# Performance work log

Hardware: AMD Instinct MI355X
Metric: run time of the kernel (lower is better)

## Reference

```python
import jax, jax.numpy as jnp
import numpy as np
from jax import lax

C, H, W, A = 256, 128, 128, 9
STRIDE = 16
BIG_NEG = -1e9
IOU_THR = 0.7
MIN_SIZE = 16.0


def _make_anchors(h, w, stride):
    scales = np.array([128.0, 256.0, 512.0])
    ratios = np.array([0.5, 1.0, 2.0])
    ah = (scales[:, None] * np.sqrt(ratios)[None, :]).reshape(-1)  # (9,)
    aw = (scales[:, None] / np.sqrt(ratios)[None, :]).reshape(-1)
    cy = (np.arange(h) + 0.5) * stride
    cx = (np.arange(w) + 0.5) * stride
    CY, CX = np.meshgrid(cy, cx, indexing='ij')
    anch = np.stack([
        np.broadcast_to(CY[..., None], (h, w, A)),
        np.broadcast_to(CX[..., None], (h, w, A)),
        np.broadcast_to(ah, (h, w, A)),
        np.broadcast_to(aw, (h, w, A)),
    ], axis=-1)  # (h, w, A, 4) as [cy, cx, h, w]
    return anch.reshape(h, w, A * 4).astype(np.float32)


def _conv(x, w, b):
    y = lax.conv_general_dilated(x, w, (1, 1), 'SAME',
                                 dimension_numbers=('NCHW', 'OIHW', 'NCHW'))
    return y + b[None, :, None, None]


def _iou_one_vs_all(box, boxes):
    # box: (4,) [y1,x1,y2,x2]; boxes: (N,4)
    yy1 = jnp.maximum(box[0], boxes[:, 0])
    xx1 = jnp.maximum(box[1], boxes[:, 1])
    yy2 = jnp.minimum(box[2], boxes[:, 2])
    xx2 = jnp.minimum(box[3], boxes[:, 3])
    inter = jnp.clip(yy2 - yy1, 0.0) * jnp.clip(xx2 - xx1, 0.0)
    a1 = (box[2] - box[0]) * (box[3] - box[1])
    a2 = (boxes[:, 2] - boxes[:, 0]) * (boxes[:, 3] - boxes[:, 1])
    return inter / (a1 + a2 - inter + 1e-9)


def _nms(boxes, scores, k):
    # Greedy NMS: k sequential argmax+suppress steps (jit-safe, fixed shapes).
    def step(s, _):
        i = jnp.argmax(s)
        valid = s[i] > BIG_NEG / 2
        iou = _iou_one_vs_all(boxes[i], boxes)
        s2 = jnp.where(iou > IOU_THR, BIG_NEG, s).at[i].set(BIG_NEG)
        return s2, (i, valid)
    _, (idxs, valids) = lax.scan(step, scores, None, length=k)
    return idxs, valids


def _rpn_forward(x, anchors, conv1_w, conv1_b, cls_w, cls_b, bbox_w, bbox_b,
                 image_h, image_w, before_n, after_n):
    h = jax.nn.relu(_conv(x, conv1_w, conv1_b))
    scores = jax.nn.sigmoid(_conv(h, cls_w, cls_b))          # (1, A, H, W)
    regs = _conv(h, bbox_w, bbox_b)                          # (1, 4A, H, W)
    scores_nhwc = jnp.transpose(scores, (0, 2, 3, 1))        # (1, H, W, A)
    regs_nhwc = jnp.transpose(regs, (0, 2, 3, 1))            # (1, H, W, 4A)

    anchors_flat = anchors.reshape(-1, 4)                    # (N, 4) [cy,cx,h,w]
    s_flat = scores_nhwc.reshape(-1)                         # (N,)
    d_flat = lax.stop_gradient(regs_nhwc.reshape(-1, 4))     # detach, as in torch

    # bbox decode (means=0, stds=1)
    cy = anchors_flat[:, 0] + d_flat[:, 0] * anchors_flat[:, 2]
    cx = anchors_flat[:, 1] + d_flat[:, 1] * anchors_flat[:, 3]
    bh = anchors_flat[:, 2] * jnp.exp(d_flat[:, 2])
    bw = anchors_flat[:, 3] * jnp.exp(d_flat[:, 3])
    props = jnp.stack([cy - 0.5 * bh, cx - 0.5 * bw,
                       cy + 0.5 * bh, cx + 0.5 * bw], axis=-1)  # (N,4) corners

    order = jnp.argsort(-s_flat)[:before_n]                  # top-N by score desc
    boxes = props[order]
    s_top = s_flat[order]

    # clip to image
    boxes = jnp.stack([jnp.clip(boxes[:, 0], 0.0),
                       jnp.clip(boxes[:, 1], 0.0),
                       jnp.minimum(boxes[:, 2], float(image_h)),
                       jnp.minimum(boxes[:, 3], float(image_w))], axis=-1)

    # size filter (>=16 in both dims): mask out via BIG_NEG score
    bh2 = boxes[:, 2] - boxes[:, 0]
    bw2 = boxes[:, 3] - boxes[:, 1]
    s_top = jnp.where((bh2 >= MIN_SIZE) & (bw2 >= MIN_SIZE), s_top, BIG_NEG)

    idxs, valids = _nms(boxes, s_top, after_n)
    out_boxes = boxes[idxs] * valids[:, None].astype(boxes.dtype)  # (after_n, 4)
    return scores_nhwc, regs_nhwc, out_boxes


def setup_inputs() -> dict:
    key = jax.random.key(0)
    k = jax.random.split(key, 4)
    x = jax.random.normal(k[0], (1, C, H, W), jnp.float32)
    conv1_w = 0.01 * jax.random.normal(k[1], (C, C, 3, 3), jnp.float32)
    conv1_b = jnp.zeros((C,), jnp.float32)
    cls_w = 0.01 * jax.random.normal(k[2], (A, C, 1, 1), jnp.float32)
    cls_b = jnp.zeros((A,), jnp.float32)
    bbox_w = 0.01 * jax.random.normal(k[3], (4 * A, C, 1, 1), jnp.float32)
    bbox_b = jnp.zeros((4 * A,), jnp.float32)
    anchors = jnp.asarray(_make_anchors(H, W, STRIDE))
    anchors_valid_map = jnp.ones((H, W, A), jnp.int32)
    return dict(x=x, anchors=anchors, conv1_w=conv1_w, conv1_b=conv1_b,
                cls_w=cls_w, cls_b=cls_b, bbox_w=bbox_w, bbox_b=bbox_b,
                anchors_valid_map=anchors_valid_map,
                image_h=2048, image_w=2048,
                before_proposal_num=6000, after_proposal_num=300)


def reference(x, anchors, conv1_w, conv1_b, cls_w, cls_b, bbox_w, bbox_b,
              anchors_valid_map, image_h, image_w,
              before_proposal_num, after_proposal_num):
    # exclude_edge_proposals=False -> anchors_valid_map unused (no boolean mask)
    return _rpn_forward(x, anchors, conv1_w, conv1_b, cls_w, cls_b,
                        bbox_w, bbox_b, image_h, image_w,
                        before_proposal_num, after_proposal_num)
```

## Files before the change

### kernel.cpp

```cpp
#include <hip/hip_runtime.h>
#include <cmath>

#define NN 147456
#define NPX 16384
#define NB 6000
#define NA 300
#define MW 94
#define EXPB 0x3FEu

__global__ __launch_bounds__(256) void prep_w_k(const float* __restrict__ w, float* __restrict__ wT2,
                                                unsigned int* __restrict__ ghist, unsigned int* __restrict__ cnt,
                                                unsigned long long* __restrict__ flagsG) {
    if (blockIdx.x == 0) {
        for (int i = threadIdx.x; i < 4096; i += 256) ghist[i] = 0;
        if (threadIdx.x == 0) cnt[0] = 0;
        if (threadIdx.x < MW) flagsG[threadIdx.x] = 0ULL;
    }
    int idx = blockIdx.x * 256 + threadIdx.x;
    if (idx >= 2304 * 256) return;
    int co = idx / 2304;
    int k  = idx - co * 2304;
    wT2[k * 256 + co] = w[idx];
}

__global__ __launch_bounds__(128, 2) void conv3_k(const float* __restrict__ x, const float* __restrict__ wT2,
                                                  const float* __restrict__ bias, double* __restrict__ h64) {
    __shared__ double xd[800];
    __shared__ __align__(16) float wl[4608];
    const int bx = blockIdx.x;
    const int tile = ((bx >> 5) << 3) | (bx & 7);
    const int g = (bx >> 3) & 3;
    const int ty0 = (tile >> 4) << 3;
    const int tx0 = (tile & 15) << 3;
    const int tid = threadIdx.x;
    const int qc = tid & 15;
    const int py = tid >> 4;
    const int wv = tid >> 6;
    const int lane = tid & 63;

    int xga[7]; bool xin[7], xwr[7];
    #pragma unroll
    for (int r = 0; r < 7; ++r) {
        int l = tid + r * 128;
        xwr[r] = (l < 800);
        int ci = l / 100; int rem = l - ci * 100;
        int rr = rem / 10; int cc = rem - rr * 10;
        int gy = ty0 + rr - 1, gx = tx0 + cc - 1;
        xin[r] = xwr[r] && gy >= 0 && gy < 128 && gx >= 0 && gx < 128;
        xga[r] = ci * NPX + gy * 128 + gx;
    }
    const float* wbase = wT2 + (g << 6);
    int wsrc[9];
    #pragma unroll
    for (int r = 0; r < 9; ++r) {
        int f = wv * 64 + lane + r * 128;
        wsrc[r] = ((f >> 4) << 8) + ((f & 15) << 2);
    }

    double acc[4][8];
    #pragma unroll
    for (int a = 0; a < 4; ++a)
        #pragma unroll
        for (int b = 0; b < 8; ++b) acc[a][b] = 0.0;

    float xf[7];
    #pragma unroll
    for (int r = 0; r < 7; ++r) { float v = 0.f; if (xin[r]) v = x[xga[r]]; xf[r] = v; }

    for (int ch = 0; ch < 32; ++ch) {
        const float* wp = wbase + ch * 18432;
        __syncthreads();
        #pragma unroll
        for (int r = 0; r < 7; ++r) {
            int l = tid + r * 128;
            if (l < 800) xd[l] = (double)xf[r];
        }
        #pragma unroll
        for (int r = 0; r < 9; ++r) {
            __builtin_amdgcn_global_load_lds(
                (const __attribute__((address_space(1))) unsigned int*)(wp + wsrc[r]),
                (__attribute__((address_space(3))) unsigned int*)&wl[(wv * 64 + r * 128) << 2],
                16, 0, 0);
        }
        __syncthreads();
        if (ch < 31) {
            const int xoff = (ch + 1) * (8 * NPX);
            #pragma unroll
            for (int r = 0; r < 7; ++r) { float v = 0.f; if (xin[r]) v = x[xoff + xga[r]]; xf[r] = v; }
        }
        for (int ci = 0; ci < 8; ++ci) {
            #pragma unroll
            for (int dy = 0; dy < 3; ++dy) {
                double xr[10];
                #pragma unroll
                for (int jj = 0; jj < 5; ++jj) {
                    double2 t = *(const double2*)&xd[ci * 100 + (py + dy) * 10 + 2 * jj];
                    xr[2 * jj] = t.x; xr[2 * jj + 1] = t.y;
                }
                #pragma unroll
                for (int dx = 0; dx < 3; ++dx) {
                    float4 wq = *(const float4*)&wl[((ci * 9 + dy * 3 + dx) << 6) + (qc << 2)];
                    double wvv[4];
                    wvv[0] = (double)wq.x; wvv[1] = (double)wq.y;
                    wvv[2] = (double)wq.z; wvv[3] = (double)wq.w;
                    #pragma unroll
                    for (int co = 0; co < 4; ++co)
                        #pragma unroll
                        for (int p = 0; p < 8; ++p)
                            acc[co][p] = fma(wvv[co], xr[p + dx], acc[co][p]);
                }
            }
        }
    }
    const int oy = ty0 + py;
    #pragma unroll
    for (int co = 0; co < 4; ++co) {
        int oc = (g << 6) + (qc << 2) + co;
        double b = (double)bias[oc];
        #pragma unroll
        for (int p = 0; p < 8; ++p) {
            double v = acc[co][p] + b;
            h64[(size_t)oc * NPX + oy * 128 + tx0 + p] = v > 0.0 ? v : 0.0;
        }
    }
}

__global__ __launch_bounds__(1024) void heads_k(const double* __restrict__ h64,
        const float* __restrict__ cls_w, const float* __restrict__ cls_b,
        const float* __restrict__ bbox_w, const float* __restrict__ bbox_b,
        float* __restrict__ out_scores, float* __restrict__ out_regs,
        double* __restrict__ scores64, double* __restrict__ regs64,
        unsigned int* __restrict__ ghist) {
    __shared__ float wlh[45 * 256];
    __shared__ unsigned int lh[4096];
    const int tid = threadIdx.x;
    for (int l = tid; l < 45 * 256; l += 1024)
        wlh[l] = (l < 2304) ? cls_w[l] : bbox_w[l - 2304];
    for (int i = tid; i < 4096; i += 1024) lh[i] = 0;
    __syncthreads();
    const int w = tid >> 6;
    const int lane = tid & 63;
    const int px = blockIdx.x * 64 + lane;
    const int o0 = w, o1 = w + 16, o2 = w + 32;
    const bool has2 = (o2 < 45);
    double a0 = 0.0, a1 = 0.0, a2 = 0.0;
    const float* w0 = wlh + o0 * 256;
    const float* w1 = wlh + o1 * 256;
    const float* w2 = wlh + (has2 ? o2 : 0) * 256;
    for (int c = 0; c < 256; ++c) {
        double hv = h64[(size_t)c * NPX + px];
        a0 = fma(hv, (double)w0[c], a0);
        a1 = fma(hv, (double)w1[c], a1);
        if (has2) a2 = fma(hv, (double)w2[c], a2);
    }
    auto emit = [&](int o, double acc) {
        if (o < 9) {
            acc += (double)cls_b[o];
            double s = 1.0 / (1.0 + exp(-acc));
            out_scores[px * 9 + o] = (float)s;
            scores64[px * 9 + o] = s;
            unsigned long long bits = (unsigned long long)__double_as_longlong(s);
            if ((unsigned int)(bits >> 52) == EXPB)
                atomicAdd(&lh[(unsigned int)(bits >> 40) & 0xFFFu], 1u);
        } else {
            acc += (double)bbox_b[o - 9];
            out_regs[px * 36 + (o - 9)] = (float)acc;
            regs64[px * 36 + (o - 9)] = acc;
        }
    };
    emit(o0, a0);
    emit(o1, a1);
    if (has2) emit(o2, a2);
    __syncthreads();
    for (int i = tid; i < 4096; i += 1024) {
        unsigned int v = lh[i];
        if (v) atomicAdd(&ghist[i], v);
    }
}

__global__ __launch_bounds__(1024) void gather_k(const double* __restrict__ s64, const unsigned int* __restrict__ ghist,
                                                 unsigned int* __restrict__ counter, unsigned int* __restrict__ cand,
                                                 unsigned long long* __restrict__ ckey) {
    __shared__ unsigned int lcnt, lbase, cutSh;
    const int tid = threadIdx.x;
    if (tid == 0) lcnt = 0;
    if (tid < 64) {
        const int lane = tid;
        unsigned int v[64];
        #pragma unroll
        for (int j = 0; j < 64; ++j) v[j] = ghist[j * 64 + lane];
        unsigned int Tl = 0;
        #pragma unroll
        for (int j = 0; j < 64; ++j) {
            unsigned int s = v[j];
            #pragma unroll
            for (int d = 1; d < 64; d <<= 1) s += __shfl_xor(s, d);
            if (lane == j) Tl = s;
        }
        unsigned int Suf = Tl;
        #pragma unroll
        for (int d = 1; d < 64; d <<= 1) { unsigned int o = __shfl_down(Suf, d); if (lane < 64 - d) Suf += o; }
        unsigned long long m = __ballot(Suf >= (unsigned int)NB);
        if (m == 0ULL) {
            if (lane == 0) cutSh = 0;
        } else {
            const int jstar = 63 - __builtin_clzll(m);
            const unsigned int above_rows = (jstar < 63) ? __shfl(Suf, jstar + 1) : 0u;
            unsigned int hrow = 0;
            #pragma unroll
            for (int j = 0; j < 64; ++j) if (j == jstar) hrow = v[j];
            unsigned int D = hrow;
            #pragma unroll
            for (int d = 1; d < 64; d <<= 1) { unsigned int o = __shfl_down(D, d); if (lane < 64 - d) D += o; }
            unsigned long long m2 = __ballot(above_rows + D >= (unsigned int)NB);
            const int lstar = 63 - __builtin_clzll(m2);
            if (lane == 0) cutSh = (unsigned int)(64 * jstar + lstar);
        }
    }
    __syncthreads();
    const unsigned int T24 = (EXPB << 12) | cutSh;
    const int gid = blockIdx.x * 1024 + tid;
    unsigned long long bits = (unsigned long long)__double_as_longlong(s64[gid]);
    unsigned int k24 = (unsigned int)(bits >> 40);
    unsigned int pos = 0;
    const bool take = (k24 >= T24);
    if (take) pos = atomicAdd(&lcnt, 1u);
    __syncthreads();
    if (tid == 0) lbase = lcnt ? atomicAdd(counter, lcnt) : 0u;
    __syncthreads();
    if (take) {
        unsigned int p = lbase + pos;
        if (p < 8192) { cand[p] = (unsigned int)gid; ckey[p] = bits; }
    }
}

__global__ __launch_bounds__(256) void rank2_k(const unsigned long long* __restrict__ ckey,
        const unsigned int* __restrict__ cand, const unsigned int* __restrict__ counter,
        const float* __restrict__ anchors, const double* __restrict__ r64,
        double* __restrict__ boxes64, unsigned long long* __restrict__ flagsG) {
    int M = (int)*counter; if (M > 8192) M = 8192;
    const int wid = (blockIdx.x * 256 + threadIdx.x) >> 6;
    const int lane = threadIdx.x & 63;
    if (wid >= M) return;
    const unsigned long long myk = ckey[wid];
    const unsigned int myv = cand[wid];
    int cntv = 0;
    int l = lane;
    for (; l + 192 < M; l += 256) {
        unsigned long long k0 = ckey[l], k1 = ckey[l + 64], k2 = ckey[l + 128], k3 = ckey[l + 192];
        unsigned int v0 = cand[l], v1 = cand[l + 64], v2 = cand[l + 128], v3 = cand[l + 192];
        cntv += (k0 > myk || (k0 == myk && v0 < myv));
        cntv += (k1 > myk || (k1 == myk && v1 < myv));
        cntv += (k2 > myk || (k2 == myk && v2 < myv));
        cntv += (k3 > myk || (k3 == myk && v3 < myv));
    }
    for (; l < M; l += 64) {
        unsigned long long kk = ckey[l];
        unsigned int vv = cand[l];
        cntv += (kk > myk || (kk == myk && vv < myv));
    }
    #pragma unroll
    for (int dd = 32; dd; dd >>= 1) cntv += __shfl_down(cntv, dd);
    if (lane == 0 && cntv < NB) {
        const int rk = cntv;
        const int i = (int)myv;
        const int px = i / 9, a = i - 9 * px;
        const float* an = anchors + px * 36 + a * 4;
        const double* d = r64 + px * 36 + a * 4;
        const double acy = (double)an[0], acx = (double)an[1], ah = (double)an[2], aw = (double)an[3];
        const double cy = acy + d[0] * ah;
        const double cx = acx + d[1] * aw;
        const double bh = ah * exp(d[2]);
        const double bw = aw * exp(d[3]);
        double y1 = cy - 0.5 * bh, x1 = cx - 0.5 * bw;
        double y2 = cy + 0.5 * bh, x2 = cx + 0.5 * bw;
        y1 = fmax(y1, 0.0); x1 = fmax(x1, 0.0);
        y2 = fmin(y2, 2048.0); x2 = fmin(x2, 2048.0);
        boxes64[rk * 4 + 0] = y1; boxes64[rk * 4 + 1] = x1;
        boxes64[rk * 4 + 2] = y2; boxes64[rk * 4 + 3] = x2;
        if (((y2 - y1) >= 16.0) && ((x2 - x1) >= 16.0))
            atomicOr(&flagsG[rk >> 6], 1ULL << (rk & 63));
    }
}

__global__ __launch_bounds__(64) void iou_k(const double* __restrict__ boxes64, unsigned long long* __restrict__ mask) {
    const int bi = blockIdx.x, bj = blockIdx.y;
    const int t = threadIdx.x;
    const int i = bi * 64 + t;
    if (bj < bi) {
        if (i < NB) mask[(size_t)i * MW + bj] = 0ULL;
        return;
    }
    __shared__ double jb[64][4];
    const int j0 = bj * 64;
    const int jn = min(64, NB - j0);
    if (t < jn) {
        jb[t][0] = boxes64[(j0 + t) * 4 + 0];
        jb[t][1] = boxes64[(j0 + t) * 4 + 1];
        jb[t][2] = boxes64[(j0 + t) * 4 + 2];
        jb[t][3] = boxes64[(j0 + t) * 4 + 3];
    }
    __syncthreads();
    if (i >= NB) return;
    const double y1 = boxes64[i * 4 + 0], x1 = boxes64[i * 4 + 1];
    const double y2 = boxes64[i * 4 + 2], x2 = boxes64[i * 4 + 3];
    const double a1 = (y2 - y1) * (x2 - x1);
    unsigned long long wbits = 0ULL;
    for (int jj = 0; jj < jn; ++jj) {
        const int j = j0 + jj;
        if (j <= i) continue;
        const double yy1 = fmax(y1, jb[jj][0]);
        const double xx1 = fmax(x1, jb[jj][1]);
        const double yy2 = fmin(y2, jb[jj][2]);
        const double xx2 = fmin(x2, jb[jj][3]);
        const double ih = fmax(yy2 - yy1, 0.0);
        const double iw = fmax(xx2 - xx1, 0.0);
        const double inter = ih * iw;
        const double a2 = (jb[jj][2] - jb[jj][0]) * (jb[jj][3] - jb[jj][1]);
        const double iou = inter / (a1 + a2 - inter + 1e-9);
        if (iou > 0.7) wbits |= (1ULL << jj);
    }
    mask[(size_t)i * MW + bj] = wbits;
}

__global__ __launch_bounds__(64) void nms_k(const double* __restrict__ boxes64,
                                            const unsigned long long* __restrict__ flagsG,
                                            const unsigned long long* __restrict__ mask, float* __restrict__ out_boxes) {
    __shared__ unsigned long long flags[MW], supp[MW];
    const int lane = threadIdx.x;
    for (int w = lane; w < MW; w += 64) { flags[w] = flagsG[w]; supp[w] = 0ULL; }
    __syncthreads();
    int nk = 0;
    for (int w = 0; w < MW && nk < NA; ++w) {
        unsigned long long done = 0ULL;
        const bool loWord = (w < 64);
        const int holder = loWord ? w : (w - 64);
        for (;;) {
            if (nk >= NA) break;
            unsigned long long avail = flags[w] & ~supp[w] & ~done;
            if (!avail) break;
            int b[16]; int n = 0;
            unsigned long long t = avail;
            #pragma unroll
            for (int q = 0; q < 16; ++q) {
                if (t) { b[q] = __builtin_ctzll(t); t &= t - 1; n = q + 1; }
                else   { b[q] = 0; }
            }
            unsigned long long dmask = 0ULL;
            #pragma unroll
            for (int q = 0; q < 16; ++q) if (q < n) dmask |= 1ULL << b[q];
            done |= dmask;
            unsigned long long r0[16], r1[16];
            #pragma unroll
            for (int q = 0; q < 16; ++q) {
                int cq = w * 64 + ((q < n) ? b[q] : b[0]);
                r0[q] = mask[(size_t)cq * MW + lane];
                r1[q] = (lane + 64 < MW) ? mask[(size_t)cq * MW + lane + 64] : 0ULL;
            }
            double bxv;
            {
                int q = lane >> 2;
                int cq = w * 64 + ((q < n) ? b[q] : b[0]);
                bxv = boxes64[(size_t)cq * 4 + (lane & 3)];
            }
            unsigned km[15];
            #pragma unroll
            for (int qp = 0; qp < 15; ++qp) {
                unsigned m = 0;
                if (qp + 1 < n) {
                    unsigned long long wordq = __shfl(loWord ? r0[qp] : r1[qp], holder);
                    #pragma unroll
                    for (int q = 1; q < 16; ++q)
                        if (q > qp) m |= ((unsigned)((wordq >> b[q]) & 1ULL)) << q;
                }
                km[qp] = m;
            }
            unsigned selm = 1u;
            #pragma unroll
            for (int q = 1; q < 16; ++q) {
                if (q < n) {
                    unsigned kb = 0;
                    #pragma unroll
                    for (int qp = 0; qp < 15; ++qp)
                        if (qp < q) kb |= ((km[qp] >> q) & 1u) << qp;
                    if ((kb & selm) == 0u) selm |= (1u << q);
                }
            }
            int outpos[16]; int nsel = 0;
            #pragma unroll
            for (int q = 0; q < 16; ++q) { outpos[q] = nk + nsel; if (q < n && ((selm >> q) & 1u)) ++nsel; }
            {
                int q = lane >> 2;
                if (q < n && ((selm >> q) & 1u) && outpos[q] < NA)
                    out_boxes[outpos[q] * 4 + (lane & 3)] = (float)bxv;
            }
            unsigned long long o0 = 0ULL, o1 = 0ULL;
            #pragma unroll
            for (int q = 0; q < 16; ++q)
                if (q < n && ((selm >> q) & 1u)) { o0 |= r0[q]; o1 |= r1[q]; }
            supp[lane] |= o0;
            if (lane + 64 < MW) supp[lane + 64] |= o1;
            nk += nsel;
        }
    }
    for (int k = nk; k < NA; ++k)
        if (lane < 4) out_boxes[k * 4 + lane] = 0.f;
}

extern "C" void kernel_launch(void* const* d_in, const int* in_sizes, int n_in,
                              void* d_out, int out_size, void* d_ws, size_t ws_size,
                              hipStream_t stream) {
    (void)in_sizes; (void)n_in; (void)out_size; (void)ws_size;
    const float* x       = (const float*)d_in[0];
    const float* anchors = (const float*)d_in[1];
    const float* conv1_w = (const float*)d_in[2];
    const float* conv1_b = (const float*)d_in[3];
    const float* cls_w   = (const float*)d_in[4];
    const float* cls_b   = (const float*)d_in[5];
    const float* bbox_w  = (const float*)d_in[6];
    const float* bbox_b  = (const float*)d_in[7];
    float* out = (float*)d_out;
    float* out_scores = out;
    float* out_regs   = out + NN;
    float* out_boxes  = out + NN * 5;

    char* ws = (char*)d_ws;
    unsigned int*       cand    = (unsigned int*)(ws + 256);
    double*             boxes64 = (double*)(ws + 33024);
    unsigned long long* mask    = (unsigned long long*)(ws + 273024);
    unsigned long long* ckey    = (unsigned long long*)(ws + 273024);
    double* h64 = (double*)(ws + 0);
    float*  wT2 = (float*)(ws + 33554432);
    double* s64 = (double*)(ws + 35913728);
    double* r64 = (double*)(ws + 37093376);
    unsigned int*       ghist  = (unsigned int*)(ws + 41811968);
    unsigned int*       cnt    = (unsigned int*)(ws + 41828352);
    unsigned long long* flagsG = (unsigned long long*)(ws + 41828608);

    prep_w_k<<<2304, 256, 0, stream>>>(conv1_w, wT2, ghist, cnt, flagsG);
    conv3_k<<<1024, 128, 0, stream>>>(x, wT2, conv1_b, h64);
    heads_k<<<256, 1024, 0, stream>>>(h64, cls_w, cls_b, bbox_w, bbox_b,
                                      out_scores, out_regs, s64, r64, ghist);
    gather_k<<<144, 1024, 0, stream>>>(s64, ghist, cnt, cand, ckey);
    rank2_k<<<2048, 256, 0, stream>>>(ckey, cand, cnt, anchors, r64, boxes64, flagsG);
    iou_k<<<dim3(MW, MW), 64, 0, stream>>>(boxes64, mask);
    nms_k<<<1, 64, 0, stream>>>(boxes64, flagsG, mask, out_boxes);
}
```

Baseline: 602.7 us.

## Shrink heads kernel to 4 waves with 11-12 outputs each and scalar weight loads

The 1x1 head kernel now runs 256 threads per block instead of 1024, and each wave computes 11 or 12 output channels instead of about 3. Weights are read straight from global memory using a wave-uniform index, so they can go through scalar loads, and the shared-memory weight staging is removed. Each h64 value loaded is reused across more outputs, which cuts the number of times the h tensor is read. The trade-off is fewer waves per block and more registers per thread, which lowers the parallelism available to hide memory latency.

Result: slower. 654.8 us (+8.6%).

```diff
diff --git a/kernel.cpp b/kernel.cpp
--- a/kernel.cpp
+++ b/kernel.cpp
@@ -125,54 +125,52 @@
     }
 }
 
-__global__ __launch_bounds__(1024) void heads_k(const double* __restrict__ h64,
+__global__ __launch_bounds__(256) void heads_k(const double* __restrict__ h64,
         const float* __restrict__ cls_w, const float* __restrict__ cls_b,
         const float* __restrict__ bbox_w, const float* __restrict__ bbox_b,
         float* __restrict__ out_scores, float* __restrict__ out_regs,
         double* __restrict__ scores64, double* __restrict__ regs64,
         unsigned int* __restrict__ ghist) {
-    __shared__ float wlh[45 * 256];
     __shared__ unsigned int lh[4096];
     const int tid = threadIdx.x;
-    for (int l = tid; l < 45 * 256; l += 1024)
-        wlh[l] = (l < 2304) ? cls_w[l] : bbox_w[l - 2304];
-    for (int i = tid; i < 4096; i += 1024) lh[i] = 0;
-    __syncthreads();
-    const int w = tid >> 6;
+    for (int i = tid; i < 4096; i += 256) lh[i] = 0;
+    __syncthreads();
+    const int wu = __builtin_amdgcn_readfirstlane(tid >> 6);
     const int lane = tid & 63;
     const int px = blockIdx.x * 64 + lane;
-    const int o0 = w, o1 = w + 16, o2 = w + 32;
-    const bool has2 = (o2 < 45);
-    double a0 = 0.0, a1 = 0.0, a2 = 0.0;
-    const float* w0 = wlh + o0 * 256;
-    const float* w1 = wlh + o1 * 256;
-    const float* w2 = wlh + (has2 ? o2 : 0) * 256;
+    double acc[12];
+    #pragma unroll
+    for (int k = 0; k < 12; ++k) acc[k] = 0.0;
     for (int c = 0; c < 256; ++c) {
-        double hv = h64[(size_t)c * NPX + px];
-        a0 = fma(hv, (double)w0[c], a0);
-        a1 = fma(hv, (double)w1[c], a1);
-        if (has2) a2 = fma(hv, (double)w2[c], a2);
-    }
-    auto emit = [&](int o, double acc) {
+        const double hv = h64[(size_t)c * NPX + px];
+        #pragma unroll
+        for (int k = 0; k < 11; ++k) {
+            const int o = wu + 4 * k;
+            const float wgt = (o < 9) ? cls_w[o * 256 + c] : bbox_w[(o - 9) * 256 + c];
+            acc[k] = fma(hv, (double)wgt, acc[k]);
+        }
+        if (wu == 0) acc[11] = fma(hv, (double)bbox_w[35 * 256 + c], acc[11]);
+    }
+    auto emit = [&](int o, double a) {
         if (o < 9) {
-            acc += (double)cls_b[o];
-            double s = 1.0 / (1.0 + exp(-acc));
+            a += (double)cls_b[o];
+            double s = 1.0 / (1.0 + exp(-a));
             out_scores[px * 9 + o] = (float)s;
             scores64[px * 9 + o] = s;
             unsigned long long bits = (unsigned long long)__double_as_longlong(s);
             if ((unsigned int)(bits >> 52) == EXPB)
                 atomicAdd(&lh[(unsigned int)(bits >> 40) & 0xFFFu], 1u);
         } else {
-            acc += (double)bbox_b[o - 9];
-            out_regs[px * 36 + (o - 9)] = (float)acc;
-            regs64[px * 36 + (o - 9)] = acc;
+            a += (double)bbox_b[o - 9];
+            out_regs[px * 36 + (o - 9)] = (float)a;
+            regs64[px * 36 + (o - 9)] = a;
         }
     };
-    emit(o0, a0);
-    emit(o1, a1);
-    if (has2) emit(o2, a2);
-    __syncthreads();
-    for (int i = tid; i < 4096; i += 1024) {
+    #pragma unroll
+    for (int k = 0; k < 11; ++k) emit(wu + 4 * k, acc[k]);
+    if (wu == 0) emit(44, acc[11]);
+    __syncthreads();
+    for (int i = tid; i < 4096; i += 256) {
         unsigned int v = lh[i];
         if (v) atomicAdd(&ghist[i], v);
     }
@@ -439,8 +437,8 @@
 
     prep_w_k<<<2304, 256, 0, stream>>>(conv1_w, wT2, ghist, cnt, flagsG);
     conv3_k<<<1024, 128, 0, stream>>>(x, wT2, conv1_b, h64);
-    heads_k<<<256, 1024, 0, stream>>>(h64, cls_w, cls_b, bbox_w, bbox_b,
-                                      out_scores, out_regs, s64, r64, ghist);
+    heads_k<<<256, 256, 0, stream>>>(h64, cls_w, cls_b, bbox_w, bbox_b,
+                                     out_scores, out_regs, s64, r64, ghist);
     gather_k<<<144, 1024, 0, stream>>>(s64, ghist, cnt, cand, ckey);
     rank2_k<<<2048, 256, 0, stream>>>(ckey, cand, cnt, anchors, r64, boxes64, flagsG);
     iou_k<<<dim3(MW, MW), 64, 0, stream>>>(boxes64, mask);
```

## Split conv3 input-channel reduction across two blocks with fp64 atomic accumulation

Applied to the files above, without the earlier changes.

Doubles the conv3 grid by splitting the 256 input channels into two halves, with each half's partial sums accumulated into h64 via double atomicAdd. h64 is zeroed with a memset beforehand. The bias add and ReLU move into the heads kernel's load of h64. This targets underutilised compute units from the small grid, at the cost of an extra 32MB memset and atomic write traffic.

Result: slower. 852.8 us (+41.5%).

```diff
diff --git a/kernel.cpp b/kernel.cpp
--- a/kernel.cpp
+++ b/kernel.cpp
@@ -24,12 +24,14 @@
 }
 
 __global__ __launch_bounds__(128, 2) void conv3_k(const float* __restrict__ x, const float* __restrict__ wT2,
-                                                  const float* __restrict__ bias, double* __restrict__ h64) {
+                                                  double* __restrict__ h64) {
     __shared__ double xd[800];
     __shared__ __align__(16) float wl[4608];
     const int bx = blockIdx.x;
-    const int tile = ((bx >> 5) << 3) | (bx & 7);
-    const int g = (bx >> 3) & 3;
+    const int ks = bx >> 10;
+    const int bxl = bx & 1023;
+    const int tile = ((bxl >> 5) << 3) | (bxl & 7);
+    const int g = (bxl >> 3) & 3;
     const int ty0 = (tile >> 4) << 3;
     const int tx0 = (tile & 15) << 3;
     const int tid = threadIdx.x;
@@ -38,15 +40,14 @@
     const int wv = tid >> 6;
     const int lane = tid & 63;
 
-    int xga[7]; bool xin[7], xwr[7];
+    int xga[7]; bool xin[7];
     #pragma unroll
     for (int r = 0; r < 7; ++r) {
         int l = tid + r * 128;
-        xwr[r] = (l < 800);
         int ci = l / 100; int rem = l - ci * 100;
         int rr = rem / 10; int cc = rem - rr * 10;
         int gy = ty0 + rr - 1, gx = tx0 + cc - 1;
-        xin[r] = xwr[r] && gy >= 0 && gy < 128 && gx >= 0 && gx < 128;
+        xin[r] = (l < 800) && gy >= 0 && gy < 128 && gx >= 0 && gx < 128;
         xga[r] = ci * NPX + gy * 128 + gx;
     }
     const float* wbase = wT2 + (g << 6);
@@ -63,11 +64,15 @@
         #pragma unroll
         for (int b = 0; b < 8; ++b) acc[a][b] = 0.0;
 
+    const int ch0 = ks * 16;
     float xf[7];
-    #pragma unroll
-    for (int r = 0; r < 7; ++r) { float v = 0.f; if (xin[r]) v = x[xga[r]]; xf[r] = v; }
-
-    for (int ch = 0; ch < 32; ++ch) {
+    {
+        const int xoff = ch0 * (8 * NPX);
+        #pragma unroll
+        for (int r = 0; r < 7; ++r) { float v = 0.f; if (xin[r]) v = x[xoff + xga[r]]; xf[r] = v; }
+    }
+
+    for (int ch = ch0; ch < ch0 + 16; ++ch) {
         const float* wp = wbase + ch * 18432;
         __syncthreads();
         #pragma unroll
@@ -83,7 +88,7 @@
                 16, 0, 0);
         }
         __syncthreads();
-        if (ch < 31) {
+        if (ch < ch0 + 15) {
             const int xoff = (ch + 1) * (8 * NPX);
             #pragma unroll
             for (int r = 0; r < 7; ++r) { float v = 0.f; if (xin[r]) v = x[xoff + xga[r]]; xf[r] = v; }
@@ -116,16 +121,14 @@
     #pragma unroll
     for (int co = 0; co < 4; ++co) {
         int oc = (g << 6) + (qc << 2) + co;
-        double b = (double)bias[oc];
-        #pragma unroll
-        for (int p = 0; p < 8; ++p) {
-            double v = acc[co][p] + b;
-            h64[(size_t)oc * NPX + oy * 128 + tx0 + p] = v > 0.0 ? v : 0.0;
-        }
+        #pragma unroll
+        for (int p = 0; p < 8; ++p)
+            atomicAdd(&h64[(size_t)oc * NPX + oy * 128 + tx0 + p], acc[co][p]);
     }
 }
 
 __global__ __launch_bounds__(1024) void heads_k(const double* __restrict__ h64,
+        const float* __restrict__ conv_b,
         const float* __restrict__ cls_w, const float* __restrict__ cls_b,
         const float* __restrict__ bbox_w, const float* __restrict__ bbox_b,
         float* __restrict__ out_scores, float* __restrict__ out_regs,
@@ -148,7 +151,7 @@
     const float* w1 = wlh + o1 * 256;
     const float* w2 = wlh + (has2 ? o2 : 0) * 256;
     for (int c = 0; c < 256; ++c) {
-        double hv = h64[(size_t)c * NPX + px];
+        double hv = fmax(h64[(size_t)c * NPX + px] + (double)conv_b[c], 0.0);
         a0 = fma(hv, (double)w0[c], a0);
         a1 = fma(hv, (double)w1[c], a1);
         if (has2) a2 = fma(hv, (double)w2[c], a2);
@@ -437,9 +440,10 @@
     unsigned int*       cnt    = (unsigned int*)(ws + 41828352);
     unsigned long long* flagsG = (unsigned long long*)(ws + 41828608);
 
+    hipMemsetAsync(h64, 0, 33554432, stream);
     prep_w_k<<<2304, 256, 0, stream>>>(conv1_w, wT2, ghist, cnt, flagsG);
-    conv3_k<<<1024, 128, 0, stream>>>(x, wT2, conv1_b, h64);
-    heads_k<<<256, 1024, 0, stream>>>(h64, cls_w, cls_b, bbox_w, bbox_b,
+    conv3_k<<<2048, 128, 0, stream>>>(x, wT2, h64);
+    heads_k<<<256, 1024, 0, stream>>>(h64, conv1_b, cls_w, cls_b, bbox_w, bbox_b,
                                       out_scores, out_regs, s64, r64, ghist);
     gather_k<<<144, 1024, 0, stream>>>(s64, ghist, cnt, cand, ckey);
     rank2_k<<<2048, 256, 0, stream>>>(ckey, cand, cnt, anchors, r64, boxes64, flagsG);
```
